# Performance work log

Measured on AMD Instinct MI355X. Metric: run time of the kernel, lower is better.

## Reference

```python
import jax, jax.numpy as jnp
import numpy as np

N_NODES = 100000
N_EDGES = 3200000
N_GRAPHS = 1024
D_IN, D_HID, N_CLASSES = 128, 64, 10


def setup_inputs() -> dict:
    key = jax.random.key(0)
    ks = jax.random.split(key, 12)
    x = jax.random.normal(ks[0], (N_NODES, D_IN), dtype=jnp.float32)
    edge_index = jax.random.randint(ks[1], (2, N_EDGES), 0, N_NODES, dtype=jnp.int64)
    batch = jnp.sort(jax.random.randint(ks[2], (N_NODES,), 0, N_GRAPHS, dtype=jnp.int64))
    def w(k, shape, fan_in):
        return (jax.random.normal(k, shape, dtype=jnp.float32) / np.sqrt(fan_in)).astype(jnp.float32)
    return {
        "x": x,
        "edge_index": edge_index,
        "batch": batch,
        "W1": w(ks[3], (D_IN, D_HID), D_IN),  "b1": jnp.zeros((D_HID,), jnp.float32),
        "W2": w(ks[4], (D_HID, D_HID), D_HID), "b2": jnp.zeros((D_HID,), jnp.float32),
        "W3": w(ks[5], (D_HID, D_HID), D_HID), "b3": jnp.zeros((D_HID,), jnp.float32),
        "Wl": w(ks[6], (D_HID, N_CLASSES), D_HID), "bl": jnp.zeros((N_CLASSES,), jnp.float32),
    }


def _gcn_conv(x, W, b, src, dst, n_nodes):
    # GCNConv: out = D^{-1/2} (A + I) D^{-1/2} X W + b  (symmetric norm, self-loops)
    h = x @ W  # [N, D_out] - transform first (PyG order)
    loop = jnp.arange(n_nodes, dtype=src.dtype)
    s = jnp.concatenate([src, loop])  # [E+N]
    d = jnp.concatenate([dst, loop])
    deg = jax.ops.segment_sum(jnp.ones_like(d, dtype=h.dtype), d, num_segments=n_nodes)
    dinv = jnp.where(deg > 0, jax.lax.rsqrt(deg), 0.0)
    norm = dinv[s] * dinv[d]  # [E+N]
    out = jax.ops.segment_sum(h[s] * norm[:, None], d, num_segments=n_nodes)
    return out + b


def reference(x, edge_index, batch, W1, b1, W2, b2, W3, b3, Wl, bl):
    src, dst = edge_index[0], edge_index[1]
    n = x.shape[0]
    h = jax.nn.relu(_gcn_conv(x, W1, b1, src, dst, n))
    h = jax.nn.relu(_gcn_conv(h, W2, b2, src, dst, n))
    h = _gcn_conv(h, W3, b3, src, dst, n)
    # global mean pool over graphs
    sums = jax.ops.segment_sum(h, batch, num_segments=N_GRAPHS)
    cnts = jax.ops.segment_sum(jnp.ones((n,), h.dtype), batch, num_segments=N_GRAPHS)
    g = sums / jnp.maximum(cnts, 1.0)[:, None]
    # dropout is identity in eval mode
    return g @ Wl + bl  # [N_GRAPHS, N_CLASSES]
```

## Files before the change

kernel.cpp:

```cpp
#include <hip/hip_runtime.h>
#include <hip/hip_fp16.h>

#define D_IN 128
#define D_HID 64
#define N_GRAPHS 1024
#define N_CLASSES 10

#define NPB 256
#define MAXNB 1024
#define CHUNK 16384

typedef __attribute__((ext_vector_type(8))) short bf16x8;
typedef __attribute__((ext_vector_type(4))) float f32x4;

__device__ __forceinline__ unsigned bf16_rne(float f) {
    unsigned u = __float_as_uint(f);
    return (u + 0x7FFF + ((u >> 16) & 1)) >> 16;
}

__global__ __launch_bounds__(256) void hist_buckets(const int* __restrict__ dst, int nE, int NB,
                                                    int* __restrict__ bcnt) {
    __shared__ int h[MAXNB];
    for (int i = threadIdx.x; i < NB; i += 256) h[i] = 0;
    __syncthreads();
    int stride = gridDim.x * 256;
    for (int i = blockIdx.x * 256 + threadIdx.x; i < nE; i += stride)
        atomicAdd(&h[dst[i] >> 8], 1);
    __syncthreads();
    for (int i = threadIdx.x; i < NB; i += 256) {
        int c = h[i];
        if (c) atomicAdd(&bcnt[i], c);
    }
}

__global__ __launch_bounds__(1024) void scan_buckets(const int* __restrict__ bcnt, int NB, int nE,
                                                     int* __restrict__ boff, int* __restrict__ gcur) {
    __shared__ int t[1024];
    int tid = threadIdx.x;
    int v = (tid < NB) ? bcnt[tid] : 0;
    t[tid] = v;
    __syncthreads();
    for (int off = 1; off < 1024; off <<= 1) {
        int u = (tid >= off) ? t[tid - off] : 0;
        __syncthreads();
        t[tid] += u;
        __syncthreads();
    }
    int excl = t[tid] - v;
    if (tid < NB) { boff[tid] = excl; gcur[tid] = excl; }
    if (tid == 0) boff[NB] = nE;
}

__global__ __launch_bounds__(1024) void bin_edges(const int* __restrict__ src, const int* __restrict__ dst,
                                                  int nE, int NB, int* __restrict__ gcur,
                                                  int* __restrict__ binned) {
    __shared__ int h[MAXNB];
    __shared__ int base[MAXNB];
    int c0 = blockIdx.x * CHUNK;
    int c1 = min(nE, c0 + CHUNK);
    for (int i = threadIdx.x; i < NB; i += 1024) h[i] = 0;
    __syncthreads();
    for (int i = c0 + threadIdx.x; i < c1; i += 1024) atomicAdd(&h[dst[i] >> 8], 1);
    __syncthreads();
    for (int b = threadIdx.x; b < NB; b += 1024) {
        int c = h[b];
        base[b] = c ? atomicAdd(&gcur[b], c) : 0;
        h[b] = 0;
    }
    __syncthreads();
    for (int i = c0 + threadIdx.x; i < c1; i += 1024) {
        int d = dst[i];
        int b = d >> 8;
        int r = atomicAdd(&h[b], 1);
        binned[base[b] + r] = src[i] | ((d & 255) << 17);
    }
}

__global__ __launch_bounds__(256) void build_csr(const int* __restrict__ boff,
                                                 const int* __restrict__ binned,
                                                 int n, int nE,
                                                 int* __restrict__ rowptr, float* __restrict__ dinv,
                                                 int* __restrict__ csr_src) {
    __shared__ int cnt[NPB];
    __shared__ int soff[NPB];
    __shared__ int cur[NPB];
    int b = blockIdx.x, tid = threadIdx.x;
    int nbase = b << 8;
    int e0 = boff[b], e1 = boff[b + 1];
    cnt[tid] = 0;
    __syncthreads();
    for (int i = e0 + tid; i < e1; i += 256) atomicAdd(&cnt[binned[i] >> 17], 1);
    __syncthreads();
    int v = cnt[tid];
    soff[tid] = v;
    __syncthreads();
    for (int off = 1; off < 256; off <<= 1) {
        int u = (tid >= off) ? soff[tid - off] : 0;
        __syncthreads();
        soff[tid] += u;
        __syncthreads();
    }
    int excl = soff[tid] - v;
    __syncthreads();
    soff[tid] = excl;
    cur[tid] = 0;
    int node = nbase + tid;
    if (node < n) {
        rowptr[node] = e0 + excl;
        dinv[node] = 1.0f / sqrtf((float)(cnt[tid] + 1));
    }
    if (b == 0 && tid == 0) rowptr[n] = nE;
    __syncthreads();
    for (int i = e0 + tid; i < e1; i += 256) {
        int e = binned[i];
        int ld = e >> 17;
        int r = atomicAdd(&cur[ld], 1);
        csr_src[e0 + soff[ld] + r] = e & 0x1FFFF;
    }
}

template <int K>
__global__ void pack_w(const float* __restrict__ W, short* __restrict__ hi, short* __restrict__ lo) {
    constexpr int SLOTS = (K / 32) * 4 * 64;
    for (int s = threadIdx.x; s < SLOTS; s += 256) {
        int lane = s & 63, nf = (s >> 6) & 3, ks = s >> 8;
        int fq = lane >> 4, fr = lane & 15;
#pragma unroll
        for (int j = 0; j < 8; ++j) {
            int k = ks * 32 + fq * 8 + j;
            int c = nf * 16 + fr;
            float v = W[k * 64 + c];
            unsigned hb = bf16_rne(v);
            float hf = __uint_as_float(hb << 16);
            float l = v - hf;
            hi[s * 8 + j] = (short)hb;
            lo[s * 8 + j] = (short)bf16_rne(l);
        }
    }
}

template <int K>
__global__ __launch_bounds__(256) void gemm_mfma(
    const float* __restrict__ X, const short* __restrict__ whi, const short* __restrict__ wlo,
    const float* __restrict__ bias, int relu, __half* __restrict__ H, int n) {
    constexpr int KS = K / 32;
    int wave = threadIdx.x >> 6, lane = threadIdx.x & 63;
    int fr = lane & 15, fq = lane >> 4;
    int rowbase = blockIdx.x * 64 + wave * 16;
    int rclamp = min(rowbase + fr, n - 1);
    f32x4 acc[4] = {{0,0,0,0},{0,0,0,0},{0,0,0,0},{0,0,0,0}};
#pragma unroll
    for (int ks = 0; ks < KS; ++ks) {
        const float* xp = X + (size_t)rclamp * K + ks * 32 + fq * 8;
        float xv[8];
        *(f32x4*)&xv[0] = *(const f32x4*)xp;
        *(f32x4*)&xv[4] = *(const f32x4*)(xp + 4);
        if (bias != nullptr) {
            const float* bp = bias + ks * 32 + fq * 8;
#pragma unroll
            for (int j = 0; j < 8; ++j) {
                float v = xv[j] + bp[j];
                if (relu) v = fmaxf(v, 0.0f);
                xv[j] = v;
            }
        }
        bf16x8 ahi, alo;
#pragma unroll
        for (int j = 0; j < 8; ++j) {
            unsigned hb = bf16_rne(xv[j]);
            float hf = __uint_as_float(hb << 16);
            ahi[j] = (short)hb;
            alo[j] = (short)bf16_rne(xv[j] - hf);
        }
        const short* whp = whi + (size_t)(ks * 4) * 64 * 8 + lane * 8;
        const short* wlp = wlo + (size_t)(ks * 4) * 64 * 8 + lane * 8;
#pragma unroll
        for (int nf = 0; nf < 4; ++nf) {
            bf16x8 bhi = *(const bf16x8*)(whp + nf * 512);
            bf16x8 blo = *(const bf16x8*)(wlp + nf * 512);
            acc[nf] = __builtin_amdgcn_mfma_f32_16x16x32_bf16(ahi, bhi, acc[nf], 0, 0, 0);
            acc[nf] = __builtin_amdgcn_mfma_f32_16x16x32_bf16(alo, bhi, acc[nf], 0, 0, 0);
            acc[nf] = __builtin_amdgcn_mfma_f32_16x16x32_bf16(ahi, blo, acc[nf], 0, 0, 0);
        }
    }
#pragma unroll
    for (int nf = 0; nf < 4; ++nf) {
#pragma unroll
        for (int reg = 0; reg < 4; ++reg) {
            int r = rowbase + fq * 4 + reg;
            if (r < n) H[((size_t)r << 6) + nf * 16 + fr] = __float2half(acc[nf][reg]);
        }
    }
}

__global__ __launch_bounds__(256) void gather_agg(
    const int* __restrict__ rowptr, const int* __restrict__ csr_src,
    const float* __restrict__ dinv, const __half* __restrict__ A,
    float* __restrict__ B, int n) {
    int gtid = blockIdx.x * 256 + threadIdx.x;
    int wid = gtid >> 6, lane = gtid & 63;
    int nw = (gridDim.x * 256) >> 6;
    int slot = lane >> 3, fl = lane & 7;
    for (int d = wid; d < n; d += nw) {
        float dd = dinv[d];
        int e0 = rowptr[d], e1 = rowptr[d + 1];
        float acc[8];
#pragma unroll
        for (int j = 0; j < 8; ++j) acc[j] = 0.0f;
        if (slot == 0) {
            uint4 q = *(const uint4*)(A + ((size_t)d << 6) + (fl << 3));
            const __half2* hp = (const __half2*)&q;
            float w = dd * dd;
#pragma unroll
            for (int j = 0; j < 4; ++j) {
                float2 f = __half22float2(hp[j]);
                acc[2 * j] = w * f.x;
                acc[2 * j + 1] = w * f.y;
            }
        }
        int e = e0 + slot;
        for (; e + 8 < e1; e += 16) {
            int s0 = csr_src[e], s1 = csr_src[e + 8];
            float w0 = dd * dinv[s0], w1 = dd * dinv[s1];
            uint4 q0 = *(const uint4*)(A + ((size_t)s0 << 6) + (fl << 3));
            uint4 q1 = *(const uint4*)(A + ((size_t)s1 << 6) + (fl << 3));
            const __half2* h0 = (const __half2*)&q0;
            const __half2* h1 = (const __half2*)&q1;
#pragma unroll
            for (int j = 0; j < 4; ++j) {
                float2 f0 = __half22float2(h0[j]);
                float2 f1 = __half22float2(h1[j]);
                acc[2 * j]     = fmaf(w0, f0.x, acc[2 * j]);
                acc[2 * j + 1] = fmaf(w0, f0.y, acc[2 * j + 1]);
                acc[2 * j]     = fmaf(w1, f1.x, acc[2 * j]);
                acc[2 * j + 1] = fmaf(w1, f1.y, acc[2 * j + 1]);
            }
        }
        if (e < e1) {
            int s = csr_src[e];
            float w = dd * dinv[s];
            uint4 q = *(const uint4*)(A + ((size_t)s << 6) + (fl << 3));
            const __half2* hp = (const __half2*)&q;
#pragma unroll
            for (int j = 0; j < 4; ++j) {
                float2 f = __half22float2(hp[j]);
                acc[2 * j]     = fmaf(w, f.x, acc[2 * j]);
                acc[2 * j + 1] = fmaf(w, f.y, acc[2 * j + 1]);
            }
        }
#pragma unroll
        for (int m = 8; m <= 32; m <<= 1)
#pragma unroll
            for (int j = 0; j < 8; ++j) acc[j] += __shfl_xor(acc[j], m);
        if (slot == 0) {
            float* bp = B + ((size_t)d << 6) + (fl << 3);
            *(f32x4*)bp = *(f32x4*)&acc[0];
            *(f32x4*)(bp + 4) = *(f32x4*)&acc[4];
        }
    }
}

__global__ __launch_bounds__(256) void pool_nodes(
    const float* __restrict__ B, const float* __restrict__ b3,
    const int* __restrict__ batch, float* __restrict__ sums,
    float* __restrict__ gcnt, int n, int chunk) {
    int gtid = blockIdx.x * blockDim.x + threadIdx.x;
    int wid = gtid >> 6, lane = gtid & 63;
    int start = wid * chunk;
    if (start >= n) return;
    int end = min(n, start + chunk);
    float bl3 = b3[lane];
    int curg = batch[start];
    float acc = 0.0f;
    int cl = 0;
    for (int node = start; node < end; ++node) {
        int g = batch[node];
        if (g != curg) {
            atomicAdd(&sums[((size_t)curg << 6) + lane], acc);
            if (lane == 0) atomicAdd(&gcnt[curg], (float)cl);
            acc = 0.0f; cl = 0; curg = g;
        }
        acc += B[((size_t)node << 6) + lane] + bl3;
        ++cl;
    }
    atomicAdd(&sums[((size_t)curg << 6) + lane], acc);
    if (lane == 0) atomicAdd(&gcnt[curg], (float)cl);
}

__global__ void final_linear(const float* __restrict__ sums, const float* __restrict__ gcnt,
                             const float* __restrict__ Wl, const float* __restrict__ bl,
                             float* __restrict__ out) {
    int idx = blockIdx.x * blockDim.x + threadIdx.x;
    if (idx >= N_GRAPHS * N_CLASSES) return;
    int g = idx / N_CLASSES, c = idx - g * N_CLASSES;
    float inv = 1.0f / fmaxf(gcnt[g], 1.0f);
    float acc = bl[c];
#pragma unroll
    for (int d = 0; d < D_HID; ++d)
        acc = fmaf(sums[(g << 6) + d] * inv, Wl[d * N_CLASSES + c], acc);
    out[idx] = acc;
}

extern "C" void kernel_launch(void* const* d_in, const int* in_sizes, int n_in,
                              void* d_out, int out_size, void* d_ws, size_t ws_size,
                              hipStream_t stream) {
    const float* x     = (const float*)d_in[0];
    const int*   ei    = (const int*)d_in[1];
    const int*   batch = (const int*)d_in[2];
    const float* W1 = (const float*)d_in[3];
    const float* b1 = (const float*)d_in[4];
    const float* W2 = (const float*)d_in[5];
    const float* b2 = (const float*)d_in[6];
    const float* W3 = (const float*)d_in[7];
    const float* b3 = (const float*)d_in[8];
    const float* Wl = (const float*)d_in[9];
    const float* bl = (const float*)d_in[10];

    int n = in_sizes[0] / D_IN;
    int E = in_sizes[1] / 2;
    const int* src = ei;
    const int* dst = ei + E;
    int NB = (n + NPB - 1) / NPB;

    size_t off = 0;
    auto alloc = [&](size_t bytes) {
        void* p = (char*)d_ws + off;
        off += ((bytes + 255) & ~(size_t)255);
        return p;
    };
    int*    rowptr  = (int*)alloc(((size_t)n + 1) * 4);
    int*    bcnt    = (int*)alloc(MAXNB * 4);
    int*    boff    = (int*)alloc((MAXNB + 1) * 4);
    int*    gcur    = (int*)alloc(MAXNB * 4);
    int*    binned  = (int*)alloc((size_t)E * 4);
    int*    csr_src = (int*)alloc((size_t)E * 4);
    float*  dinv    = (float*)alloc((size_t)n * 4);
    float*  B       = (float*)alloc((size_t)n * 64 * 4);
    float*  sums    = (float*)alloc(N_GRAPHS * 64 * 4);
    float*  gcnt    = (float*)alloc(N_GRAPHS * 4);
    short*  w1hi    = (short*)alloc(4 * 4 * 64 * 8 * 2);
    short*  w1lo    = (short*)alloc(4 * 4 * 64 * 8 * 2);
    short*  w2hi    = (short*)alloc(2 * 4 * 64 * 8 * 2);
    short*  w2lo    = (short*)alloc(2 * 4 * 64 * 8 * 2);
    short*  w3hi    = (short*)alloc(2 * 4 * 64 * 8 * 2);
    short*  w3lo    = (short*)alloc(2 * 4 * 64 * 8 * 2);
    __half* A       = (__half*)binned;

    int blk = 256;
    int gBin  = (E + CHUNK - 1) / CHUNK;
    int gGemm = (n + 63) / 64;

    hipMemsetAsync(bcnt, 0, MAXNB * sizeof(int), stream);
    hist_buckets<<<1024, blk, 0, stream>>>(dst, E, NB, bcnt);
    scan_buckets<<<1, 1024, 0, stream>>>(bcnt, NB, E, boff, gcur);
    bin_edges<<<gBin, 1024, 0, stream>>>(src, dst, E, NB, gcur, binned);
    build_csr<<<NB, blk, 0, stream>>>(boff, binned, n, E, rowptr, dinv, csr_src);

    pack_w<D_IN><<<1, blk, 0, stream>>>(W1, w1hi, w1lo);
    pack_w<D_HID><<<1, blk, 0, stream>>>(W2, w2hi, w2lo);
    pack_w<D_HID><<<1, blk, 0, stream>>>(W3, w3hi, w3lo);

    gemm_mfma<D_IN><<<gGemm, blk, 0, stream>>>(x, w1hi, w1lo, nullptr, 0, A, n);
    gather_agg<<<2048, blk, 0, stream>>>(rowptr, csr_src, dinv, A, B, n);

    gemm_mfma<D_HID><<<gGemm, blk, 0, stream>>>(B, w2hi, w2lo, b1, 1, A, n);
    gather_agg<<<2048, blk, 0, stream>>>(rowptr, csr_src, dinv, A, B, n);

    gemm_mfma<D_HID><<<gGemm, blk, 0, stream>>>(B, w3hi, w3lo, b2, 1, A, n);
    gather_agg<<<2048, blk, 0, stream>>>(rowptr, csr_src, dinv, A, B, n);

    hipMemsetAsync(sums, 0, (N_GRAPHS * 64 + N_GRAPHS) * sizeof(float), stream);
    {
        int waves = 256 * 256 / 64;
        int chunk = (n + waves - 1) / waves;
        pool_nodes<<<256, blk, 0, stream>>>(B, b3, batch, sums, gcnt, n, chunk);
    }
    final_linear<<<(N_GRAPHS * N_CLASSES + blk - 1) / blk, blk, 0, stream>>>(
        sums, gcnt, Wl, bl, (float*)d_out);
}
```

Measured before the change: 358.0 us.

## Fold source-side normalization into GEMM output and store aggregates in fp16

The GEMM epilogue now scales each row by dinv[src], so the gather loop just sums neighbour features. It no longer does a dependent dinv[s] lookup per edge, and the destination dinv is applied once at the end. The intermediate aggregate buffer B switches from fp32 to fp16, which halves its write and read traffic, and the later GEMMs read fp16 input. Nontemporal loads are added for streamed edge arrays. In exchange, fp16 storage of aggregates adds rounding error.

```diff
diff --git a/kernel.cpp b/kernel.cpp
--- a/kernel.cpp
+++ b/kernel.cpp
@@ -25,7 +25,7 @@
     __syncthreads();
     int stride = gridDim.x * 256;
     for (int i = blockIdx.x * 256 + threadIdx.x; i < nE; i += stride)
-        atomicAdd(&h[dst[i] >> 8], 1);
+        atomicAdd(&h[__builtin_nontemporal_load(&dst[i]) >> 8], 1);
     __syncthreads();
     for (int i = threadIdx.x; i < NB; i += 256) {
         int c = h[i];
@@ -60,7 +60,8 @@
     int c1 = min(nE, c0 + CHUNK);
     for (int i = threadIdx.x; i < NB; i += 1024) h[i] = 0;
     __syncthreads();
-    for (int i = c0 + threadIdx.x; i < c1; i += 1024) atomicAdd(&h[dst[i] >> 8], 1);
+    for (int i = c0 + threadIdx.x; i < c1; i += 1024)
+        atomicAdd(&h[__builtin_nontemporal_load(&dst[i]) >> 8], 1);
     __syncthreads();
     for (int b = threadIdx.x; b < NB; b += 1024) {
         int c = h[b];
@@ -69,10 +70,11 @@
     }
     __syncthreads();
     for (int i = c0 + threadIdx.x; i < c1; i += 1024) {
-        int d = dst[i];
+        int d = __builtin_nontemporal_load(&dst[i]);
+        int s = __builtin_nontemporal_load(&src[i]);
         int b = d >> 8;
         int r = atomicAdd(&h[b], 1);
-        binned[base[b] + r] = src[i] | ((d & 255) << 17);
+        binned[base[b] + r] = s | ((d & 255) << 17);
     }
 }
 
@@ -89,7 +91,8 @@
     int e0 = boff[b], e1 = boff[b + 1];
     cnt[tid] = 0;
     __syncthreads();
-    for (int i = e0 + tid; i < e1; i += 256) atomicAdd(&cnt[binned[i] >> 17], 1);
+    for (int i = e0 + tid; i < e1; i += 256)
+        atomicAdd(&cnt[__builtin_nontemporal_load(&binned[i]) >> 17], 1);
     __syncthreads();
     int v = cnt[tid];
     soff[tid] = v;
@@ -112,7 +115,7 @@
     if (b == 0 && tid == 0) rowptr[n] = nE;
     __syncthreads();
     for (int i = e0 + tid; i < e1; i += 256) {
-        int e = binned[i];
+        int e = __builtin_nontemporal_load(&binned[i]);
         int ld = e >> 17;
         int r = atomicAdd(&cur[ld], 1);
         csr_src[e0 + soff[ld] + r] = e & 0x1FFFF;
@@ -139,10 +142,11 @@
     }
 }
 
-template <int K>
+template <int K, int INH>
 __global__ __launch_bounds__(256) void gemm_mfma(
-    const float* __restrict__ X, const short* __restrict__ whi, const short* __restrict__ wlo,
-    const float* __restrict__ bias, int relu, __half* __restrict__ H, int n) {
+    const void* __restrict__ Xv, const short* __restrict__ whi, const short* __restrict__ wlo,
+    const float* __restrict__ bias, int relu, const float* __restrict__ dinv,
+    __half* __restrict__ H, int n) {
     constexpr int KS = K / 32;
     int wave = threadIdx.x >> 6, lane = threadIdx.x & 63;
     int fr = lane & 15, fq = lane >> 4;
@@ -151,12 +155,24 @@
     f32x4 acc[4] = {{0,0,0,0},{0,0,0,0},{0,0,0,0},{0,0,0,0}};
 #pragma unroll
     for (int ks = 0; ks < KS; ++ks) {
-        const float* xp = X + (size_t)rclamp * K + ks * 32 + fq * 8;
+        int kbase = ks * 32 + fq * 8;
         float xv[8];
-        *(f32x4*)&xv[0] = *(const f32x4*)xp;
-        *(f32x4*)&xv[4] = *(const f32x4*)(xp + 4);
+        if (INH) {
+            const __half* xp = (const __half*)Xv + (size_t)rclamp * K + kbase;
+            uint4 q = *(const uint4*)xp;
+            const __half2* hp = (const __half2*)&q;
+#pragma unroll
+            for (int j = 0; j < 4; ++j) {
+                float2 f = __half22float2(hp[j]);
+                xv[2 * j] = f.x; xv[2 * j + 1] = f.y;
+            }
+        } else {
+            const float* xp = (const float*)Xv + (size_t)rclamp * K + kbase;
+            *(f32x4*)&xv[0] = *(const f32x4*)xp;
+            *(f32x4*)&xv[4] = *(const f32x4*)(xp + 4);
+        }
         if (bias != nullptr) {
-            const float* bp = bias + ks * 32 + fq * 8;
+            const float* bp = bias + kbase;
 #pragma unroll
             for (int j = 0; j < 8; ++j) {
                 float v = xv[j] + bp[j];
@@ -184,11 +200,13 @@
         }
     }
 #pragma unroll
-    for (int nf = 0; nf < 4; ++nf) {
-#pragma unroll
-        for (int reg = 0; reg < 4; ++reg) {
-            int r = rowbase + fq * 4 + reg;
-            if (r < n) H[((size_t)r << 6) + nf * 16 + fr] = __float2half(acc[nf][reg]);
+    for (int reg = 0; reg < 4; ++reg) {
+        int r = rowbase + fq * 4 + reg;
+        if (r < n) {
+            float dv = dinv[r];
+#pragma unroll
+            for (int nf = 0; nf < 4; ++nf)
+                H[((size_t)r << 6) + nf * 16 + fr] = __float2half(dv * acc[nf][reg]);
         }
     }
 }
@@ -196,13 +214,12 @@
 __global__ __launch_bounds__(256) void gather_agg(
     const int* __restrict__ rowptr, const int* __restrict__ csr_src,
     const float* __restrict__ dinv, const __half* __restrict__ A,
-    float* __restrict__ B, int n) {
+    __half* __restrict__ B, int n) {
     int gtid = blockIdx.x * 256 + threadIdx.x;
     int wid = gtid >> 6, lane = gtid & 63;
     int nw = (gridDim.x * 256) >> 6;
     int slot = lane >> 3, fl = lane & 7;
     for (int d = wid; d < n; d += nw) {
-        float dd = dinv[d];
         int e0 = rowptr[d], e1 = rowptr[d + 1];
         float acc[8];
 #pragma unroll
@@ -210,18 +227,17 @@
         if (slot == 0) {
             uint4 q = *(const uint4*)(A + ((size_t)d << 6) + (fl << 3));
             const __half2* hp = (const __half2*)&q;
-            float w = dd * dd;
 #pragma unroll
             for (int j = 0; j < 4; ++j) {
                 float2 f = __half22float2(hp[j]);
-                acc[2 * j] = w * f.x;
-                acc[2 * j + 1] = w * f.y;
+                acc[2 * j] = f.x;
+                acc[2 * j + 1] = f.y;
             }
         }
         int e = e0 + slot;
         for (; e + 8 < e1; e += 16) {
-            int s0 = csr_src[e], s1 = csr_src[e + 8];
-            float w0 = dd * dinv[s0], w1 = dd * dinv[s1];
+            int s0 = __builtin_nontemporal_load(&csr_src[e]);
+            int s1 = __builtin_nontemporal_load(&csr_src[e + 8]);
             uint4 q0 = *(const uint4*)(A + ((size_t)s0 << 6) + (fl << 3));
             uint4 q1 = *(const uint4*)(A + ((size_t)s1 << 6) + (fl << 3));
             const __half2* h0 = (const __half2*)&q0;
@@ -230,22 +246,19 @@
             for (int j = 0; j < 4; ++j) {
                 float2 f0 = __half22float2(h0[j]);
                 float2 f1 = __half22float2(h1[j]);
-                acc[2 * j]     = fmaf(w0, f0.x, acc[2 * j]);
-                acc[2 * j + 1] = fmaf(w0, f0.y, acc[2 * j + 1]);
-                acc[2 * j]     = fmaf(w1, f1.x, acc[2 * j]);
-                acc[2 * j + 1] = fmaf(w1, f1.y, acc[2 * j + 1]);
+                acc[2 * j]     += f0.x + f1.x;
+                acc[2 * j + 1] += f0.y + f1.y;
             }
         }
         if (e < e1) {
-            int s = csr_src[e];
-            float w = dd * dinv[s];
+            int s = __builtin_nontemporal_load(&csr_src[e]);
             uint4 q = *(const uint4*)(A + ((size_t)s << 6) + (fl << 3));
             const __half2* hp = (const __half2*)&q;
 #pragma unroll
             for (int j = 0; j < 4; ++j) {
                 float2 f = __half22float2(hp[j]);
-                acc[2 * j]     = fmaf(w, f.x, acc[2 * j]);
-                acc[2 * j + 1] = fmaf(w, f.y, acc[2 * j + 1]);
+                acc[2 * j]     += f.x;
+                acc[2 * j + 1] += f.y;
             }
         }
 #pragma unroll
@@ -253,15 +266,18 @@
 #pragma unroll
             for (int j = 0; j < 8; ++j) acc[j] += __shfl_xor(acc[j], m);
         if (slot == 0) {
-            float* bp = B + ((size_t)d << 6) + (fl << 3);
-            *(f32x4*)bp = *(f32x4*)&acc[0];
-            *(f32x4*)(bp + 4) = *(f32x4*)&acc[4];
+            float dd = dinv[d];
+            union { uint4 u; __half2 h[4]; } o;
+#pragma unroll
+            for (int j = 0; j < 4; ++j)
+                o.h[j] = __floats2half2_rn(dd * acc[2 * j], dd * acc[2 * j + 1]);
+            *(uint4*)(B + ((size_t)d << 6) + (fl << 3)) = o.u;
         }
     }
 }
 
 __global__ __launch_bounds__(256) void pool_nodes(
-    const float* __restrict__ B, const float* __restrict__ b3,
+    const __half* __restrict__ B, const float* __restrict__ b3,
     const int* __restrict__ batch, float* __restrict__ sums,
     float* __restrict__ gcnt, int n, int chunk) {
     int gtid = blockIdx.x * blockDim.x + threadIdx.x;
@@ -280,7 +296,7 @@
             if (lane == 0) atomicAdd(&gcnt[curg], (float)cl);
             acc = 0.0f; cl = 0; curg = g;
         }
-        acc += B[((size_t)node << 6) + lane] + bl3;
+        acc += __half2float(B[((size_t)node << 6) + lane]) + bl3;
         ++cl;
     }
     atomicAdd(&sums[((size_t)curg << 6) + lane], acc);
@@ -335,7 +351,7 @@
     int*    binned  = (int*)alloc((size_t)E * 4);
     int*    csr_src = (int*)alloc((size_t)E * 4);
     float*  dinv    = (float*)alloc((size_t)n * 4);
-    float*  B       = (float*)alloc((size_t)n * 64 * 4);
+    __half* B       = (__half*)alloc((size_t)n * 64 * 2);
     float*  sums    = (float*)alloc(N_GRAPHS * 64 * 4);
     float*  gcnt    = (float*)alloc(N_GRAPHS * 4);
     short*  w1hi    = (short*)alloc(4 * 4 * 64 * 8 * 2);
@@ -360,13 +376,13 @@
     pack_w<D_HID><<<1, blk, 0, stream>>>(W2, w2hi, w2lo);
     pack_w<D_HID><<<1, blk, 0, stream>>>(W3, w3hi, w3lo);
 
-    gemm_mfma<D_IN><<<gGemm, blk, 0, stream>>>(x, w1hi, w1lo, nullptr, 0, A, n);
+    gemm_mfma<D_IN, 0><<<gGemm, blk, 0, stream>>>(x, w1hi, w1lo, nullptr, 0, dinv, A, n);
     gather_agg<<<2048, blk, 0, stream>>>(rowptr, csr_src, dinv, A, B, n);
 
-    gemm_mfma<D_HID><<<gGemm, blk, 0, stream>>>(B, w2hi, w2lo, b1, 1, A, n);
+    gemm_mfma<D_HID, 1><<<gGemm, blk, 0, stream>>>(B, w2hi, w2lo, b1, 1, dinv, A, n);
     gather_agg<<<2048, blk, 0, stream>>>(rowptr, csr_src, dinv, A, B, n);
 
-    gemm_mfma<D_HID><<<gGemm, blk, 0, stream>>>(B, w3hi, w3lo, b2, 1, A, n);
+    gemm_mfma<D_HID, 1><<<gGemm, blk, 0, stream>>>(B, w3hi, w3lo, b2, 1, dinv, A, n);
     gather_agg<<<2048, blk, 0, stream>>>(rowptr, csr_src, dinv, A, B, n);
 
     hipMemsetAsync(sums, 0, (N_GRAPHS * 64 + N_GRAPHS) * sizeof(float), stream);
```

After: 395.2 us. 10.4% more time.
